# Kernel tuning notes

Hardware: AMD Instinct MI355X
Metric: run time of the kernel (lower is better)

## Reference

```python
import math
import jax, jax.numpy as jnp
import numpy as np

B, C_IN, H, W = 16, 384, 64, 64
CDIM, K, NSCALES, ITERS = 128, 64, 2, 3

def conv1x1(x, w, b):
    # x: [B,C,H,W], w: [O,C], b: [O]
    return jnp.einsum('bchw,oc->bohw', x, w) + b[None, :, None, None]

def mlp2(x, w1, b1, w2, b2):
    return conv1x1(jax.nn.relu(conv1x1(x, w1, b1)), w2, b2)

def log_optimal_transport(scores, dustbin, iters):
    B_, K_, N_ = scores.shape
    Z = jnp.concatenate([scores, dustbin], axis=1)  # [B,K+1,N]
    log_mu = jnp.full((B_, K_ + 1), -math.log(K_ + 1), dtype=scores.dtype)
    log_nu = jnp.full((B_, N_), -math.log(N_), dtype=scores.dtype)
    u = jnp.zeros_like(log_mu)
    v = jnp.zeros_like(log_nu)
    for _ in range(iters):
        u = log_mu - jax.nn.logsumexp(Z + v[:, None, :], axis=2)
        v = log_nu - jax.nn.logsumexp(Z + u[:, :, None], axis=1)
    return Z + u[:, :, None] + v[:, None, :]

def avg_pool2(x):
    b, c, h, w = x.shape
    return x.reshape(b, c, h // 2, 2, w // 2, 2).mean(axis=(3, 5))

def scale_branch(xs, fw1, fb1, fw2, fb2, sw1, sb1, sw2, sb2, dw1, db1, dw2, db2):
    b = xs.shape[0]
    local_feat = mlp2(xs, fw1, fb1, fw2, fb2).reshape(b, CDIM, -1)   # [B,C,N]
    score = mlp2(xs, sw1, sb1, sw2, sb2).reshape(b, K, -1)           # [B,K,N]
    dustbin = mlp2(xs, dw1, db1, dw2, db2).reshape(b, 1, -1)         # [B,1,N]
    log_p = log_optimal_transport(score, dustbin, ITERS)
    p = jnp.exp(log_p)[:, :-1, :]                                    # drop dustbin row
    p = p / (p.sum(axis=-1, keepdims=True) + 1e-8)
    out = jnp.einsum('bcn,bkn->bck', local_feat, p)                  # [B,C,K]
    out = out / jnp.clip(jnp.linalg.norm(out, axis=1, keepdims=True), 1e-12)
    return out.reshape(b, -1), local_feat

def setup_inputs():
    key = jax.random.key(0)
    ks = jax.random.split(key, 13)
    inp = {'x': jax.random.normal(ks[0], (B, C_IN, H, W), jnp.float32)}
    kidx = 1
    for s in range(NSCALES):
        for name, (o, i) in [('fw1', (512, C_IN)), ('fw2', (CDIM, 512)),
                              ('sw1', (512, C_IN)), ('sw2', (K, 512)),
                              ('dw1', (128, C_IN)), ('dw2', (1, 128))]:
            inp[f'{name}_{s}'] = 0.02 * jax.random.normal(ks[kidx % 13], (o, i), jnp.float32)
            inp[f'{name[0]}b{name[2]}_{s}'] = jnp.zeros((o,), jnp.float32)
            kidx += 1
    return inp

def reference(x,
              fw1_0, fb1_0, fw2_0, fb2_0, sw1_0, sb1_0, sw2_0, sb2_0, dw1_0, db1_0, dw2_0, db2_0,
              fw1_1, fb1_1, fw2_1, fb2_1, sw1_1, sb1_1, sw2_1, sb2_1, dw1_1, db1_1, dw2_1, db2_1):
    params = [
        (fw1_0, fb1_0, fw2_0, fb2_0, sw1_0, sb1_0, sw2_0, sb2_0, dw1_0, db1_0, dw2_0, db2_0),
        (fw1_1, fb1_1, fw2_1, fb2_1, sw1_1, sb1_1, sw2_1, sb2_1, dw1_1, db1_1, dw2_1, db2_1),
    ]
    descs = []
    xs = x
    for s in range(NSCALES):
        if s > 0:
            xs = avg_pool2(xs)
        d, _ = scale_branch(xs, *params[s])
        descs.append(d)
    g = jnp.stack(descs, axis=1).mean(axis=1)
    g = g / jnp.clip(jnp.linalg.norm(g, axis=1, keepdims=True), 1e-12)
    return g
```

## Files before the change

### kernel.cpp

```cpp
#include <hip/hip_runtime.h>
#include <math.h>

typedef __attribute__((ext_vector_type(8))) short short8;
typedef __attribute__((ext_vector_type(4))) float floatx4;

__device__ inline float bf2f(short s) {
    union { unsigned u; float f; } x; x.u = ((unsigned)(unsigned short)s) << 16; return x.f;
}
__device__ inline short f2bf(float f) {
    union { float f; unsigned u; } x; x.f = f;
    unsigned r = x.u + 0x7fff + ((x.u >> 16) & 1);
    return (short)(r >> 16);
}

struct WSet {
    const float *fw1, *fb1, *fw2, *sw1, *sb1, *sw2, *sb2, *dw1, *db1, *dw2, *db2;
};

__global__ __launch_bounds__(256) void wprep(WSet a0, WSet a1,
    short* __restrict__ W1f, short* __restrict__ W2af, short* __restrict__ W2bf,
    float* __restrict__ B1p, float* __restrict__ B2bp)
{
    const int s = blockIdx.y;
    const WSet A = s ? a1 : a0;
    W1f  += (size_t)s * 491520;
    W2af += (size_t)s * 65536;
    W2bf += (size_t)s * 98304;
    B1p  += s * 1280;
    B2bp += s * 128;
    int id = blockIdx.x * 256 + threadIdx.x;
    if (id < 491520) {
        int e = id & 7, l = (id >> 3) & 63, g = (id >> 9) & 15, rest = id >> 13;
        int kc = rest % 12, c = rest / 12;
        int m = c * 256 + g * 16 + (l & 15);
        int k = kc * 32 + (l >> 4) * 8 + e;
        float v = 0.f;
        if (m < 512) v = A.fw1[m * 384 + k];
        else if (m < 1024) v = A.sw1[(m - 512) * 384 + k];
        else if (m < 1152) v = A.dw1[(m - 1024) * 384 + k];
        W1f[id] = f2bf(v);
        return;
    }
    id -= 491520;
    if (id < 65536) {
        int e = id & 7, l = (id >> 3) & 63, g = (id >> 9) & 7, ka = id >> 12;
        int r = g * 16 + (l & 15), k = ka * 32 + (l >> 4) * 8 + e;
        W2af[id] = f2bf(A.fw2[r * 512 + k]);
        return;
    }
    id -= 65536;
    if (id < 98304) {
        int e = id & 7, l = (id >> 3) & 63, g = (id >> 9) & 7, kb = id >> 12;
        int r = g * 16 + (l & 15), krel = kb * 32 + (l >> 4) * 8 + e;
        float v = 0.f;
        if (r < 64 && krel < 512) v = A.sw2[r * 512 + krel];
        else if (r == 64 && krel >= 512 && krel < 640) v = A.dw2[krel - 512];
        W2bf[id] = f2bf(v);
        return;
    }
    id -= 98304;
    if (id < 1280) {
        float v = 0.f;
        if (id < 512) v = A.fb1[id];
        else if (id < 1024) v = A.sb1[id - 512];
        else if (id < 1152) v = A.db1[id - 1024];
        B1p[id] = v;
        return;
    }
    id -= 1280;
    if (id < 128) B2bp[id] = id < 64 ? A.sb2[id] : id == 64 ? A.db2[0] : 0.f;
}

__global__ __launch_bounds__(256) void xprep(const float* __restrict__ x,
                                             short* __restrict__ xT, short* __restrict__ x1T)
{
    __shared__ float xt[64 * 129];
    const int ip = blockIdx.x;
    const int cg = blockIdx.y;
    const int b  = blockIdx.z;
    const int t  = threadIdx.x;
    #pragma unroll
    for (int u = 0; u < 32; u++) {
        int idx = t + 256 * u;
        int c = idx >> 7, sp = idx & 127;
        xt[c * 129 + sp] = x[(((long)b * 384 + cg * 64 + c) * 64 + ip * 2 + (sp >> 6)) * 64 + (sp & 63)];
    }
    __syncthreads();
    {
        int sp = t >> 1, ch = t & 1;
        short tmp[32];
        #pragma unroll
        for (int cc = 0; cc < 32; cc++) tmp[cc] = f2bf(xt[(ch * 32 + cc) * 129 + sp]);
        short* dst = xT + ((long)b * 4096 + ip * 128 + sp) * 384 + cg * 64 + ch * 32;
        #pragma unroll
        for (int v = 0; v < 4; v++) *(short8*)(dst + v * 8) = *(short8*)(tmp + v * 8);
    }
    {
        int j1 = t >> 3, c8 = t & 7;
        short tmp[8];
        #pragma unroll
        for (int e = 0; e < 8; e++) {
            int c = c8 * 8 + e;
            float v = 0.25f * (xt[c * 129 + j1 * 2]      + xt[c * 129 + j1 * 2 + 1] +
                               xt[c * 129 + 64 + j1 * 2] + xt[c * 129 + 64 + j1 * 2 + 1]);
            tmp[e] = f2bf(v);
        }
        *(short8*)(x1T + ((long)b * 1024 + ip * 32 + j1) * 384 + cg * 64 + c8 * 8) = *(short8*)tmp;
    }
}

__global__ __launch_bounds__(256, 2) void fused_mlp(
    const short* __restrict__ W1f_, const float* __restrict__ B1p_,
    const short* __restrict__ W2af_, const float* __restrict__ fb2_0, const float* __restrict__ fb2_1,
    const short* __restrict__ W2bf_, const float* __restrict__ B2bp_,
    const short* __restrict__ xT, const short* __restrict__ x1T,
    float* __restrict__ feat0, float* __restrict__ feat1,
    short* __restrict__ Eg0, short* __restrict__ Eg1,
    float* __restrict__ pu0, float* __restrict__ pu1)
{
    __shared__ short xs[12 * 2048];
    __shared__ short hs[8 * 2048];
    const int tid = threadIdx.x;
    const int wid = tid >> 6, lane = tid & 63;
    const int l15 = lane & 15, q = lane >> 4;
    const int bx = blockIdx.x, b = blockIdx.y;
    const int sc = bx >= 64;
    const int tile = sc ? bx - 64 : bx;
    const int N = sc ? 1024 : 4096;
    const int n0 = tile * 64;
    const short* XT = sc ? x1T : xT;
    const short* W1f = W1f_ + (size_t)sc * 491520;
    const float* B1p = B1p_ + sc * 1280;
    const short* W2af = W2af_ + (size_t)sc * 65536;
    const short* W2bf = W2bf_ + (size_t)sc * 98304;
    const float* fb2 = sc ? fb2_1 : fb2_0;
    const float* B2bp = B2bp_ + sc * 128;
    float* feat = (sc ? feat1 : feat0) + (long)b * 128 * N;
    short* Eg = (sc ? Eg1 : Eg0) + (long)b * 65 * N;
    float* pu = sc ? pu1 : pu0;
    const int npart = sc ? 16 : 64;

    {
        const int n = tid >> 2;
        const int c0 = (tid & 3) * 12;
        const short* src = XT + ((long)b * N + n0 + n) * 384 + c0 * 8;
        const int jj = n >> 4, nl = n & 15;
        #pragma unroll
        for (int i = 0; i < 12; i++) {
            int c = c0 + i;
            int kc = c >> 2, qq = c & 3;
            *(short8*)(xs + kc * 2048 + jj * 512 + ((qq << 4) | nl) * 8) =
                *(const short8*)(src + i * 8);
        }
    }
    __syncthreads();

    floatx4 acc2[4][4];
    #pragma unroll
    for (int i = 0; i < 4; i++)
        #pragma unroll
        for (int j = 0; j < 4; j++) acc2[i][j] = floatx4{0.f, 0.f, 0.f, 0.f};

    auto phase2 = [&](int pc) {
        if (pc < 2) {
            const short* WA = W2af + (size_t)pc * 32768;
            short8 hb[2][4], wa0[2], wa1[2];
            #pragma unroll
            for (int j = 0; j < 4; j++) hb[0][j] = *(short8*)(hs + j * 512 + lane * 8);
            wa0[0] = *(const short8*)(WA + (2 * wid) * 512 + lane * 8);
            wa1[0] = *(const short8*)(WA + (2 * wid + 1) * 512 + lane * 8);
            #pragma unroll
            for (int kc2 = 0; kc2 < 8; kc2++) {
                short8 bfr[4];
                #pragma unroll
                for (int j = 0; j < 4; j++) bfr[j] = hb[kc2 & 1][j];
                short8 aA = wa0[kc2 & 1], aB = wa1[kc2 & 1];
                if (kc2 + 1 < 8) {
                    #pragma unroll
                    for (int j = 0; j < 4; j++)
                        hb[(kc2 + 1) & 1][j] = *(short8*)(hs + (kc2 + 1) * 2048 + j * 512 + lane * 8);
                    wa0[(kc2 + 1) & 1] = *(const short8*)(WA + ((kc2 + 1) * 8 + 2 * wid) * 512 + lane * 8);
                    wa1[(kc2 + 1) & 1] = *(const short8*)(WA + ((kc2 + 1) * 8 + 2 * wid + 1) * 512 + lane * 8);
                }
                #pragma unroll
                for (int j = 0; j < 4; j++) {
                    acc2[0][j] = __builtin_amdgcn_mfma_f32_16x16x32_bf16(aA, bfr[j], acc2[0][j], 0, 0, 0);
                    acc2[1][j] = __builtin_amdgcn_mfma_f32_16x16x32_bf16(aB, bfr[j], acc2[1][j], 0, 0, 0);
                }
            }
        } else {
            const short* WB = W2bf + (size_t)(pc - 2) * 32768;
            short8 hb[2][4], wc[2], wd[2];
            #pragma unroll
            for (int j = 0; j < 4; j++) hb[0][j] = *(short8*)(hs + j * 512 + lane * 8);
            wc[0] = *(const short8*)(WB + wid * 512 + lane * 8);
            wd[0] = *(const short8*)(WB + 4 * 512 + lane * 8);
            #pragma unroll
            for (int kc2 = 0; kc2 < 8; kc2++) {
                short8 bfr[4];
                #pragma unroll
                for (int j = 0; j < 4; j++) bfr[j] = hb[kc2 & 1][j];
                short8 aC = wc[kc2 & 1], aD = wd[kc2 & 1];
                if (kc2 + 1 < 8) {
                    #pragma unroll
                    for (int j = 0; j < 4; j++)
                        hb[(kc2 + 1) & 1][j] = *(short8*)(hs + (kc2 + 1) * 2048 + j * 512 + lane * 8);
                    wc[(kc2 + 1) & 1] = *(const short8*)(WB + ((kc2 + 1) * 8 + wid) * 512 + lane * 8);
                    wd[(kc2 + 1) & 1] = *(const short8*)(WB + ((kc2 + 1) * 8 + 4) * 512 + lane * 8);
                }
                #pragma unroll
                for (int j = 0; j < 4; j++)
                    acc2[2][j] = __builtin_amdgcn_mfma_f32_16x16x32_bf16(aC, bfr[j], acc2[2][j], 0, 0, 0);
                if (wid == 0) {
                    #pragma unroll
                    for (int j = 0; j < 4; j++)
                        acc2[3][j] = __builtin_amdgcn_mfma_f32_16x16x32_bf16(aD, bfr[j], acc2[3][j], 0, 0, 0);
                }
            }
        }
    };

    for (int c = 0; c < 5; c++) {
        floatx4 acc1[4][4];
        #pragma unroll
        for (int i = 0; i < 4; i++)
            #pragma unroll
            for (int j = 0; j < 4; j++) acc1[i][j] = floatx4{0.f, 0.f, 0.f, 0.f};
        const short* Wb = W1f + (long)c * 98304;
        short8 abuf[2][4], bbuf[2][4];
        #pragma unroll
        for (int i = 0; i < 4; i++) {
            abuf[0][i] = *(const short8*)(Wb + (wid * 4 + i) * 512 + lane * 8);
            abuf[1][i] = *(const short8*)(Wb + (16 + wid * 4 + i) * 512 + lane * 8);
        }
        #pragma unroll
        for (int j = 0; j < 4; j++) bbuf[0][j] = *(short8*)(xs + j * 512 + lane * 8);
        #pragma unroll
        for (int kc = 0; kc < 12; kc++) {
            short8 ac[4], bc[4];
            #pragma unroll
            for (int i = 0; i < 4; i++) ac[i] = abuf[kc & 1][i];
            #pragma unroll
            for (int j = 0; j < 4; j++) bc[j] = bbuf[kc & 1][j];
            if (kc + 2 < 12) {
                #pragma unroll
                for (int i = 0; i < 4; i++)
                    abuf[kc & 1][i] = *(const short8*)(Wb + ((kc + 2) * 16 + wid * 4 + i) * 512 + lane * 8);
            }
            if (kc + 1 < 12) {
                #pragma unroll
                for (int j = 0; j < 4; j++)
                    bbuf[(kc + 1) & 1][j] = *(short8*)(xs + (kc + 1) * 2048 + j * 512 + lane * 8);
            }
            #pragma unroll
            for (int i = 0; i < 4; i++)
                #pragma unroll
                for (int j = 0; j < 4; j++)
                    acc1[i][j] = __builtin_amdgcn_mfma_f32_16x16x32_bf16(ac[i], bc[j], acc1[i][j], 0, 0, 0);
        }
        if (c > 0) phase2(c - 1);
        __syncthreads();
        #pragma unroll
        for (int i = 0; i < 4; i++) {
            const int kc2 = wid * 2 + (i >> 1);
            const int qf = (i & 1) * 2 + (q >> 1);
            const int e0 = 4 * (q & 1);
            const int mrow = c * 256 + wid * 64 + i * 16 + q * 4;
            float bw[4];
            #pragma unroll
            for (int rr = 0; rr < 4; rr++) bw[rr] = B1p[mrow + rr];
            #pragma unroll
            for (int j = 0; j < 4; j++) {
                short pk[4];
                #pragma unroll
                for (int rr = 0; rr < 4; rr++)
                    pk[rr] = f2bf(fmaxf(acc1[i][j][rr] + bw[rr], 0.f));
                *(unsigned long long*)(hs + kc2 * 2048 + j * 512 + ((qf << 4) | l15) * 8 + e0) =
                    *(unsigned long long*)pk;
            }
        }
        __syncthreads();
    }
    phase2(4);

    #pragma unroll
    for (int slot = 0; slot < 2; slot++) {
        int row0 = (2 * wid + slot) * 16 + q * 4;
        #pragma unroll
        for (int rr = 0; rr < 4; rr++) {
            float bv = fb2[row0 + rr];
            #pragma unroll
            for (int j = 0; j < 4; j++)
                feat[(long)(row0 + rr) * N + n0 + 16 * j + l15] = acc2[slot][j][rr] + bv;
        }
    }
    __syncthreads();
    float* puld = (float*)hs;
    #pragma unroll
    for (int rr = 0; rr < 4; rr++) {
        int row = wid * 16 + q * 4 + rr;
        float bv = B2bp[row];
        float s = 0.f;
        #pragma unroll
        for (int j = 0; j < 4; j++) {
            float e = expf(acc2[2][j][rr] + bv);
            Eg[(long)row * N + n0 + 16 * j + l15] = f2bf(e);
            s += e;
        }
        s += __shfl_xor(s, 1); s += __shfl_xor(s, 2);
        s += __shfl_xor(s, 4); s += __shfl_xor(s, 8);
        if (l15 == 0) puld[row] = s;
    }
    if (wid == 0) {
        #pragma unroll
        for (int rr = 0; rr < 4; rr++) {
            int row = 64 + q * 4 + rr;
            bool valid = (row == 64);
            float bv = B2bp[64];
            float s = 0.f;
            #pragma unroll
            for (int j = 0; j < 4; j++) {
                float e = expf(acc2[3][j][rr] + bv);
                if (valid) {
                    Eg[(long)64 * N + n0 + 16 * j + l15] = f2bf(e);
                    s += e;
                }
            }
            s += __shfl_xor(s, 1); s += __shfl_xor(s, 2);
            s += __shfl_xor(s, 4); s += __shfl_xor(s, 8);
            if (valid && l15 == 0) puld[64] = s;
        }
    }
    __syncthreads();
    if (tid < 65)
        pu[((long)b * npart + tile) * 65 + tid] = puld[tid];
}

__global__ __launch_bounds__(256) void sk_step(
    const short* __restrict__ Eg0, const short* __restrict__ Eg1,
    const float* __restrict__ pin0, const float* __restrict__ pin1,
    float* __restrict__ pout0, float* __restrict__ pout1, int nin0, int nin1)
{
    __shared__ short Es[65 * 264];
    __shared__ float evs[256];
    __shared__ float eus[65];
    const int t = threadIdx.x;
    const int bx = blockIdx.x, b = blockIdx.y;
    const int sc = bx >= 16;
    const int chunk = sc ? bx - 16 : bx;
    const int N = sc ? 1024 : 4096;
    const float invN = sc ? (1.0f / 1024.0f) : (1.0f / 4096.0f);
    const int n0 = chunk * 256;
    const short* Eb = (sc ? Eg1 : Eg0) + (long)b * 65 * N;
    const float* pin = sc ? pin1 : pin0;
    const int nin = sc ? nin1 : nin0;
    float* pout = sc ? pout1 : pout0;
    const int nout = sc ? 4 : 16;
    if (t < 65) {
        float s = 0.f;
        for (int ch = 0; ch < nin; ch++) s += pin[((long)b * nin + ch) * 65 + t];
        eus[t] = (1.0f / 65.0f) / s;
    }
    for (int it = t; it < 2080; it += 256) {
        int k = it >> 5, n8 = it & 31;
        *(short8*)(Es + k * 264 + n8 * 8) = *(const short8*)(Eb + (long)k * N + n0 + n8 * 8);
    }
    __syncthreads();
    float sv = 0.f;
    #pragma unroll 4
    for (int k = 0; k < 65; k++) sv += bf2f(Es[k * 264 + t]) * eus[k];
    evs[t] = invN / sv;
    __syncthreads();
    const int wid = t >> 6, lane = t & 63;
    for (int k = wid; k < 65; k += 4) {
        const short* er = Es + k * 264 + lane * 4;
        float4 v4 = *(const float4*)&evs[lane * 4];
        float s = bf2f(er[0]) * v4.x + bf2f(er[1]) * v4.y + bf2f(er[2]) * v4.z + bf2f(er[3]) * v4.w;
        #pragma unroll
        for (int off = 32; off >= 1; off >>= 1) s += __shfl_xor(s, off);
        if (lane == 0) pout[((long)b * nout + chunk) * 65 + k] = s;
    }
}

__global__ __launch_bounds__(256) void sk_desc(
    const short* __restrict__ Eg0, const short* __restrict__ Eg1,
    const float* __restrict__ pin0, const float* __restrict__ pin1,
    const float* __restrict__ feat0, const float* __restrict__ feat1,
    float* __restrict__ part0, float* __restrict__ part1, int nin0, int nin1)
{
    __shared__ short Es[65 * 264];
    __shared__ float eus[65];
    const int t = threadIdx.x;
    const int bx = blockIdx.x, b = blockIdx.y;
    const int sc = bx >= 16;
    const int chunk = sc ? bx - 16 : bx;
    const int N = sc ? 1024 : 4096;
    const float invN = sc ? (1.0f / 1024.0f) : (1.0f / 4096.0f);
    const int nch = sc ? 4 : 16;
    const int n0 = chunk * 256;
    const short* Eb = (sc ? Eg1 : Eg0) + (long)b * 65 * N;
    const float* pin = sc ? pin1 : pin0;
    const int nin = sc ? nin1 : nin0;
    const float* fb = (sc ? feat1 : feat0) + (long)b * 128 * N;
    float* part = sc ? part1 : part0;
    if (t < 65) {
        float s = 0.f;
        for (int ch = 0; ch < nin; ch++) s += pin[((long)b * nin + ch) * 65 + t];
        eus[t] = (1.0f / 65.0f) / s;
    }
    for (int it = t; it < 2080; it += 256) {
        int k = it >> 5, n8 = it & 31;
        *(short8*)(Es + k * 264 + n8 * 8) = *(const short8*)(Eb + (long)k * N + n0 + n8 * 8);
    }
    __syncthreads();
    float sv = 0.f;
    #pragma unroll 4
    for (int k = 0; k < 65; k++) sv += bf2f(Es[k * 264 + t]) * eus[k];
    float evt = invN / sv;
    #pragma unroll 4
    for (int k = 0; k < 64; k++)
        Es[k * 264 + t] = f2bf(bf2f(Es[k * 264 + t]) * eus[k] * evt);
    __syncthreads();
    const int wid = t >> 6, lane = t & 63;
    const int l15 = lane & 15, q = lane >> 4;
    float* pb = part + ((long)b * nch + chunk) * 8256;
    for (int k = wid; k < 64; k += 4) {
        const short* er = Es + k * 264 + lane * 4;
        float s = bf2f(er[0]) + bf2f(er[1]) + bf2f(er[2]) + bf2f(er[3]);
        #pragma unroll
        for (int off = 32; off >= 1; off >>= 1) s += __shfl_xor(s, off);
        if (lane == 0) pb[8192 + k] = s;
    }
    floatx4 acc[2][4];
    #pragma unroll
    for (int mt = 0; mt < 2; mt++)
        #pragma unroll
        for (int nt = 0; nt < 4; nt++) acc[mt][nt] = floatx4{0.f, 0.f, 0.f, 0.f};
    #pragma unroll 2
    for (int ks = 0; ks < 8; ks++) {
        short8 ah[2], al[2];
        #pragma unroll
        for (int mt = 0; mt < 2; mt++) {
            const float* fp = fb + (long)(wid * 32 + mt * 16 + l15) * N + n0 + ks * 32 + q * 8;
            float4 v0 = *(const float4*)fp;
            float4 v1 = *(const float4*)(fp + 4);
            float va[8] = {v0.x, v0.y, v0.z, v0.w, v1.x, v1.y, v1.z, v1.w};
            short hh[8], ll[8];
            #pragma unroll
            for (int e = 0; e < 8; e++) {
                short h = f2bf(va[e]);
                hh[e] = h;
                ll[e] = f2bf(va[e] - bf2f(h));
            }
            ah[mt] = *(short8*)hh;
            al[mt] = *(short8*)ll;
        }
        #pragma unroll
        for (int nt = 0; nt < 4; nt++) {
            short8 bfr = *(short8*)(Es + (nt * 16 + l15) * 264 + ks * 32 + q * 8);
            #pragma unroll
            for (int mt = 0; mt < 2; mt++) {
                acc[mt][nt] = __builtin_amdgcn_mfma_f32_16x16x32_bf16(al[mt], bfr, acc[mt][nt], 0, 0, 0);
                acc[mt][nt] = __builtin_amdgcn_mfma_f32_16x16x32_bf16(ah[mt], bfr, acc[mt][nt], 0, 0, 0);
            }
        }
    }
    #pragma unroll
    for (int mt = 0; mt < 2; mt++)
        #pragma unroll
        for (int nt = 0; nt < 4; nt++)
            #pragma unroll
            for (int rr = 0; rr < 4; rr++)
                pb[(wid * 32 + mt * 16 + q * 4 + rr) * 64 + nt * 16 + l15] = acc[mt][nt][rr];
}

__global__ __launch_bounds__(256) void desc_reduce(
    const float* __restrict__ part0, const float* __restrict__ part1,
    float* __restrict__ desc0, float* __restrict__ desc1, int b0)
{
    __shared__ float cred[4][8];
    const int bx = blockIdx.x, b = blockIdx.y;
    const int sc = bx >= 4;
    const int kg = (bx & 3) * 16;
    const int nch = sc ? 4 : 16;
    const float* pb = (sc ? part1 : part0) + (long)b * nch * 8256;
    float* desc = sc ? desc1 : desc0;
    const int t = threadIdx.x;
    const int c = t & 127, kh = t >> 7;
    float a[8], rs[8];
    #pragma unroll
    for (int j = 0; j < 8; j++) { a[j] = 0.f; rs[j] = 0.f; }
    for (int ch = 0; ch < nch; ch++) {
        const float* p = pb + (long)ch * 8256;
        #pragma unroll
        for (int j = 0; j < 8; j++) a[j] += p[c * 64 + kg + kh * 8 + j];
        #pragma unroll
        for (int j = 0; j < 8; j++) rs[j] += p[8192 + kg + kh * 8 + j];
    }
    float sq[8];
    #pragma unroll
    for (int j = 0; j < 8; j++) {
        a[j] *= 1.0f / (rs[j] + 1e-8f);
        sq[j] = a[j] * a[j];
    }
    #pragma unroll
    for (int off = 32; off >= 1; off >>= 1)
        #pragma unroll
        for (int j = 0; j < 8; j++) sq[j] += __shfl_xor(sq[j], off);
    if ((t & 63) == 0) {
        #pragma unroll
        for (int j = 0; j < 8; j++) cred[t >> 6][j] = sq[j];
    }
    __syncthreads();
    float* d = desc + (long)(b0 + b) * 8192;
    #pragma unroll
    for (int j = 0; j < 8; j++) {
        float tot = cred[kh * 2][j] + cred[kh * 2 + 1][j];
        float inv = 1.0f / fmaxf(sqrtf(tot), 1e-12f);
        d[c * 64 + kg + kh * 8 + j] = a[j] * inv;
    }
}

__global__ __launch_bounds__(256) void final_kernel(const float* __restrict__ desc0,
                                                    const float* __restrict__ desc1,
                                                    float* __restrict__ out)
{
    __shared__ float red[4];
    const int b = blockIdx.x;
    const float* d0 = desc0 + (long)b * 8192;
    const float* d1 = desc1 + (long)b * 8192;
    float s = 0;
    for (int i = threadIdx.x; i < 8192; i += 256) {
        float t = (d0[i] + d1[i]) * 0.5f; s += t * t;
    }
    const int wave = threadIdx.x >> 6, lane = threadIdx.x & 63;
    #pragma unroll
    for (int off = 32; off >= 1; off >>= 1) s += __shfl_xor(s, off);
    if (lane == 0) red[wave] = s;
    __syncthreads();
    float tot = red[0] + red[1] + red[2] + red[3];
    float inv = 1.0f / fmaxf(sqrtf(tot), 1e-12f);
    for (int i = threadIdx.x; i < 8192; i += 256)
        out[(long)b * 8192 + i] = (d0[i] + d1[i]) * 0.5f * inv;
}

extern "C" void kernel_launch(void* const* d_in, const int* in_sizes, int n_in,
                              void* d_out, int out_size, void* d_ws, size_t ws_size,
                              hipStream_t stream)
{
    (void)in_sizes; (void)n_in; (void)out_size;
    const float* x = (const float*)d_in[0];
    WSet ws2[2];
    const float* fb2p[2];
    for (int s = 0; s < 2; s++) {
        int o = 1 + s * 12;
        ws2[s].fw1 = (const float*)d_in[o + 0];  ws2[s].fb1 = (const float*)d_in[o + 1];
        ws2[s].fw2 = (const float*)d_in[o + 2];  fb2p[s]    = (const float*)d_in[o + 3];
        ws2[s].sw1 = (const float*)d_in[o + 4];  ws2[s].sb1 = (const float*)d_in[o + 5];
        ws2[s].sw2 = (const float*)d_in[o + 6];  ws2[s].sb2 = (const float*)d_in[o + 7];
        ws2[s].dw1 = (const float*)d_in[o + 8];  ws2[s].db1 = (const float*)d_in[o + 9];
        ws2[s].dw2 = (const float*)d_in[o + 10]; ws2[s].db2 = (const float*)d_in[o + 11];
    }

    const size_t fixed = ((size_t)2*491520*2 + 2*65536*2 + 2*98304*2
                        + 2*1280*4 + 2*128*4 + (size_t)2*16*8192*4) + (1 << 16);
    const size_t perb = (size_t)4096*384*2 + (size_t)1024*384*2
                      + (size_t)128*4096*4 + (size_t)128*1024*4
                      + (size_t)65*4096*2 + (size_t)65*1024*2
                      + (size_t)(64+16)*65*4 + (size_t)(16+4)*65*4
                      + (size_t)16*8256*4 + (size_t)4*8256*4 + 8192;
    int CB = 4;
    const int cand[3] = {16, 8, 4};
    for (int ci = 0; ci < 3; ci++)
        if (fixed + (size_t)cand[ci] * perb <= ws_size) { CB = cand[ci]; break; }

    char* p = (char*)d_ws;
    auto alloc = [&](size_t bytes) -> char* {
        char* r = p; p += (bytes + 255) & ~(size_t)255; return r;
    };
    short* W1f   = (short*)alloc((size_t)2 * 491520 * 2);
    short* W2af  = (short*)alloc((size_t)2 * 65536 * 2);
    short* W2bf  = (short*)alloc((size_t)2 * 98304 * 2);
    float* B1p   = (float*)alloc((size_t)2 * 1280 * 4);
    float* B2bp  = (float*)alloc((size_t)2 * 128 * 4);
    float* desc0 = (float*)alloc((size_t)16 * 8192 * 4);
    float* desc1 = (float*)alloc((size_t)16 * 8192 * 4);
    short* xT    = (short*)alloc((size_t)CB * 4096 * 384 * 2);
    short* x1T   = (short*)alloc((size_t)CB * 1024 * 384 * 2);
    float* feat0 = (float*)alloc((size_t)CB * 128 * 4096 * 4);
    float* feat1 = (float*)alloc((size_t)CB * 128 * 1024 * 4);
    short* Eg0   = (short*)alloc((size_t)CB * 65 * 4096 * 2);
    short* Eg1   = (short*)alloc((size_t)CB * 65 * 1024 * 2);
    float* puA0  = (float*)alloc((size_t)CB * 64 * 65 * 4);
    float* puA1  = (float*)alloc((size_t)CB * 16 * 65 * 4);
    float* puB0  = (float*)alloc((size_t)CB * 16 * 65 * 4);
    float* puB1  = (float*)alloc((size_t)CB * 4 * 65 * 4);
    float* part0 = (float*)alloc((size_t)CB * 16 * 8256 * 4);
    float* part1 = (float*)alloc((size_t)CB * 4 * 8256 * 4);

    wprep<<<dim3(2566, 2), 256, 0, stream>>>(ws2[0], ws2[1], W1f, W2af, W2bf, B1p, B2bp);

    for (int b0 = 0; b0 < 16; b0 += CB) {
        xprep<<<dim3(32, 6, CB), 256, 0, stream>>>(x + (size_t)b0 * 384 * 4096, xT, x1T);
        fused_mlp<<<dim3(80, CB), 256, 0, stream>>>(
            W1f, B1p, W2af, fb2p[0], fb2p[1], W2bf, B2bp,
            xT, x1T, feat0, feat1, Eg0, Eg1, puA0, puA1);
        sk_step<<<dim3(20, CB), 256, 0, stream>>>(Eg0, Eg1, puA0, puA1, puB0, puB1, 64, 16);
        sk_step<<<dim3(20, CB), 256, 0, stream>>>(Eg0, Eg1, puB0, puB1, puA0, puA1, 16, 4);
        sk_desc<<<dim3(20, CB), 256, 0, stream>>>(Eg0, Eg1, puA0, puA1,
                                                  feat0, feat1, part0, part1, 16, 4);
        desc_reduce<<<dim3(8, CB), 256, 0, stream>>>(part0, part1, desc0, desc1, b0);
    }
    final_kernel<<<16, 256, 0, stream>>>(desc0, desc1, (float*)d_out);
}
```

Measured before the change: 470.8 us.

## Use 512-thread blocks in fused MLP and vectorize xprep loads

The fused MLP kernel now runs 8 waves per block instead of 4, with each wave computing half as many output rows, so per-wave accumulator state drops and more waves can hide latency. The phase-2 GEMM for the previous chunk is moved ahead of the phase-1 GEMM, and the LDS double-buffering of the x tiles is replaced by direct per-iteration loads. xprep now reads x with float4 loads. In exchange, several waves sit idle in the score/dustbin phase, and the launch bound of 512 threads with 4 blocks per CU may cap registers or be unreachable given the LDS footprint.

```diff
diff --git a/kernel.cpp b/kernel.cpp
--- a/kernel.cpp
+++ b/kernel.cpp
@@ -80,10 +80,12 @@
     const int b  = blockIdx.z;
     const int t  = threadIdx.x;
     #pragma unroll
-    for (int u = 0; u < 32; u++) {
+    for (int u = 0; u < 8; u++) {
         int idx = t + 256 * u;
-        int c = idx >> 7, sp = idx & 127;
-        xt[c * 129 + sp] = x[(((long)b * 384 + cg * 64 + c) * 64 + ip * 2 + (sp >> 6)) * 64 + (sp & 63)];
+        int c = idx >> 5, spq = idx & 31;
+        float4 v = *(const float4*)&x[(((long)b * 384 + cg * 64 + c) * 64 + ip * 2 + (spq >> 4)) * 64 + (spq & 15) * 4];
+        float* d = &xt[c * 129 + spq * 4];
+        d[0] = v.x; d[1] = v.y; d[2] = v.z; d[3] = v.w;
     }
     __syncthreads();
     {
@@ -109,7 +111,7 @@
     }
 }
 
-__global__ __launch_bounds__(256, 2) void fused_mlp(
+__global__ __launch_bounds__(512, 4) void fused_mlp(
     const short* __restrict__ W1f_, const float* __restrict__ B1p_,
     const short* __restrict__ W2af_, const float* __restrict__ fb2_0, const float* __restrict__ fb2_1,
     const short* __restrict__ W2bf_, const float* __restrict__ B2bp_,
@@ -141,12 +143,12 @@
     const int npart = sc ? 16 : 64;
 
     {
-        const int n = tid >> 2;
-        const int c0 = (tid & 3) * 12;
+        const int n = tid >> 3;
+        const int c0 = (tid & 7) * 6;
         const short* src = XT + ((long)b * N + n0 + n) * 384 + c0 * 8;
         const int jj = n >> 4, nl = n & 15;
         #pragma unroll
-        for (int i = 0; i < 12; i++) {
+        for (int i = 0; i < 6; i++) {
             int c = c0 + i;
             int kc = c >> 2, qq = c & 3;
             *(short8*)(xs + kc * 2048 + jj * 512 + ((qq << 4) | nl) * 8) =
@@ -155,117 +157,99 @@
     }
     __syncthreads();
 
-    floatx4 acc2[4][4];
-    #pragma unroll
-    for (int i = 0; i < 4; i++)
+    floatx4 acc2[2][4];
+    #pragma unroll
+    for (int i = 0; i < 2; i++)
         #pragma unroll
         for (int j = 0; j < 4; j++) acc2[i][j] = floatx4{0.f, 0.f, 0.f, 0.f};
 
     auto phase2 = [&](int pc) {
         if (pc < 2) {
             const short* WA = W2af + (size_t)pc * 32768;
-            short8 hb[2][4], wa0[2], wa1[2];
+            short8 hb[2][4], wa[2];
             #pragma unroll
             for (int j = 0; j < 4; j++) hb[0][j] = *(short8*)(hs + j * 512 + lane * 8);
-            wa0[0] = *(const short8*)(WA + (2 * wid) * 512 + lane * 8);
-            wa1[0] = *(const short8*)(WA + (2 * wid + 1) * 512 + lane * 8);
+            wa[0] = *(const short8*)(WA + wid * 512 + lane * 8);
             #pragma unroll
             for (int kc2 = 0; kc2 < 8; kc2++) {
                 short8 bfr[4];
                 #pragma unroll
                 for (int j = 0; j < 4; j++) bfr[j] = hb[kc2 & 1][j];
-                short8 aA = wa0[kc2 & 1], aB = wa1[kc2 & 1];
+                short8 aF = wa[kc2 & 1];
                 if (kc2 + 1 < 8) {
                     #pragma unroll
                     for (int j = 0; j < 4; j++)
                         hb[(kc2 + 1) & 1][j] = *(short8*)(hs + (kc2 + 1) * 2048 + j * 512 + lane * 8);
-                    wa0[(kc2 + 1) & 1] = *(const short8*)(WA + ((kc2 + 1) * 8 + 2 * wid) * 512 + lane * 8);
-                    wa1[(kc2 + 1) & 1] = *(const short8*)(WA + ((kc2 + 1) * 8 + 2 * wid + 1) * 512 + lane * 8);
+                    wa[(kc2 + 1) & 1] = *(const short8*)(WA + ((kc2 + 1) * 8 + wid) * 512 + lane * 8);
                 }
                 #pragma unroll
-                for (int j = 0; j < 4; j++) {
-                    acc2[0][j] = __builtin_amdgcn_mfma_f32_16x16x32_bf16(aA, bfr[j], acc2[0][j], 0, 0, 0);
-                    acc2[1][j] = __builtin_amdgcn_mfma_f32_16x16x32_bf16(aB, bfr[j], acc2[1][j], 0, 0, 0);
-                }
+                for (int j = 0; j < 4; j++)
+                    acc2[0][j] = __builtin_amdgcn_mfma_f32_16x16x32_bf16(aF, bfr[j], acc2[0][j], 0, 0, 0);
             }
         } else {
+            if (wid >= 5) return;
             const short* WB = W2bf + (size_t)(pc - 2) * 32768;
-            short8 hb[2][4], wc[2], wd[2];
+            short8 hb[2][4], we[2];
             #pragma unroll
             for (int j = 0; j < 4; j++) hb[0][j] = *(short8*)(hs + j * 512 + lane * 8);
-            wc[0] = *(const short8*)(WB + wid * 512 + lane * 8);
-            wd[0] = *(const short8*)(WB + 4 * 512 + lane * 8);
+            we[0] = *(const short8*)(WB + wid * 512 + lane * 8);
             #pragma unroll
             for (int kc2 = 0; kc2 < 8; kc2++) {
                 short8 bfr[4];
                 #pragma unroll
                 for (int j = 0; j < 4; j++) bfr[j] = hb[kc2 & 1][j];
-                short8 aC = wc[kc2 & 1], aD = wd[kc2 & 1];
+                short8 aE = we[kc2 & 1];
                 if (kc2 + 1 < 8) {
                     #pragma unroll
                     for (int j = 0; j < 4; j++)
                         hb[(kc2 + 1) & 1][j] = *(short8*)(hs + (kc2 + 1) * 2048 + j * 512 + lane * 8);
-                    wc[(kc2 + 1) & 1] = *(const short8*)(WB + ((kc2 + 1) * 8 + wid) * 512 + lane * 8);
-                    wd[(kc2 + 1) & 1] = *(const short8*)(WB + ((kc2 + 1) * 8 + 4) * 512 + lane * 8);
+                    we[(kc2 + 1) & 1] = *(const short8*)(WB + ((kc2 + 1) * 8 + wid) * 512 + lane * 8);
                 }
                 #pragma unroll
                 for (int j = 0; j < 4; j++)
-                    acc2[2][j] = __builtin_amdgcn_mfma_f32_16x16x32_bf16(aC, bfr[j], acc2[2][j], 0, 0, 0);
-                if (wid == 0) {
-                    #pragma unroll
-                    for (int j = 0; j < 4; j++)
-                        acc2[3][j] = __builtin_amdgcn_mfma_f32_16x16x32_bf16(aD, bfr[j], acc2[3][j], 0, 0, 0);
-                }
+                    acc2[1][j] = __builtin_amdgcn_mfma_f32_16x16x32_bf16(aE, bfr[j], acc2[1][j], 0, 0, 0);
             }
         }
     };
 
     for (int c = 0; c < 5; c++) {
-        floatx4 acc1[4][4];
-        #pragma unroll
-        for (int i = 0; i < 4; i++)
+        if (c > 0) phase2(c - 1);
+        floatx4 acc1[2][4];
+        #pragma unroll
+        for (int i = 0; i < 2; i++)
             #pragma unroll
             for (int j = 0; j < 4; j++) acc1[i][j] = floatx4{0.f, 0.f, 0.f, 0.f};
         const short* Wb = W1f + (long)c * 98304;
-        short8 abuf[2][4], bbuf[2][4];
-        #pragma unroll
-        for (int i = 0; i < 4; i++) {
-            abuf[0][i] = *(const short8*)(Wb + (wid * 4 + i) * 512 + lane * 8);
-            abuf[1][i] = *(const short8*)(Wb + (16 + wid * 4 + i) * 512 + lane * 8);
-        }
-        #pragma unroll
-        for (int j = 0; j < 4; j++) bbuf[0][j] = *(short8*)(xs + j * 512 + lane * 8);
+        short8 abuf[2][2];
+        #pragma unroll
+        for (int i = 0; i < 2; i++) {
+            abuf[0][i] = *(const short8*)(Wb + (wid * 2 + i) * 512 + lane * 8);
+            abuf[1][i] = *(const short8*)(Wb + (16 + wid * 2 + i) * 512 + lane * 8);
+        }
         #pragma unroll
         for (int kc = 0; kc < 12; kc++) {
-            short8 ac[4], bc[4];
-            #pragma unroll
-            for (int i = 0; i < 4; i++) ac[i] = abuf[kc & 1][i];
-            #pragma unroll
-            for (int j = 0; j < 4; j++) bc[j] = bbuf[kc & 1][j];
+            short8 ac[2], bc[4];
+            #pragma unroll
+            for (int i = 0; i < 2; i++) ac[i] = abuf[kc & 1][i];
+            #pragma unroll
+            for (int j = 0; j < 4; j++) bc[j] = *(short8*)(xs + kc * 2048 + j * 512 + lane * 8);
             if (kc + 2 < 12) {
                 #pragma unroll
-                for (int i = 0; i < 4; i++)
-                    abuf[kc & 1][i] = *(const short8*)(Wb + ((kc + 2) * 16 + wid * 4 + i) * 512 + lane * 8);
-            }
-            if (kc + 1 < 12) {
-                #pragma unroll
-                for (int j = 0; j < 4; j++)
-                    bbuf[(kc + 1) & 1][j] = *(short8*)(xs + (kc + 1) * 2048 + j * 512 + lane * 8);
-            }
-            #pragma unroll
-            for (int i = 0; i < 4; i++)
+                for (int i = 0; i < 2; i++)
+                    abuf[kc & 1][i] = *(const short8*)(Wb + ((kc + 2) * 16 + wid * 2 + i) * 512 + lane * 8);
+            }
+            #pragma unroll
+            for (int i = 0; i < 2; i++)
                 #pragma unroll
                 for (int j = 0; j < 4; j++)
                     acc1[i][j] = __builtin_amdgcn_mfma_f32_16x16x32_bf16(ac[i], bc[j], acc1[i][j], 0, 0, 0);
         }
-        if (c > 0) phase2(c - 1);
         __syncthreads();
         #pragma unroll
-        for (int i = 0; i < 4; i++) {
-            const int kc2 = wid * 2 + (i >> 1);
-            const int qf = (i & 1) * 2 + (q >> 1);
+        for (int i = 0; i < 2; i++) {
+            const int qf = i * 2 + (q >> 1);
             const int e0 = 4 * (q & 1);
-            const int mrow = c * 256 + wid * 64 + i * 16 + q * 4;
+            const int mrow = c * 256 + wid * 32 + i * 16 + q * 4;
             float bw[4];
             #pragma unroll
             for (int rr = 0; rr < 4; rr++) bw[rr] = B1p[mrow + rr];
@@ -275,7 +259,7 @@
                 #pragma unroll
                 for (int rr = 0; rr < 4; rr++)
                     pk[rr] = f2bf(fmaxf(acc1[i][j][rr] + bw[rr], 0.f));
-                *(unsigned long long*)(hs + kc2 * 2048 + j * 512 + ((qf << 4) | l15) * 8 + e0) =
+                *(unsigned long long*)(hs + wid * 2048 + j * 512 + ((qf << 4) | l15) * 8 + e0) =
                     *(unsigned long long*)pk;
             }
         }
@@ -283,35 +267,35 @@
     }
     phase2(4);
 
-    #pragma unroll
-    for (int slot = 0; slot < 2; slot++) {
-        int row0 = (2 * wid + slot) * 16 + q * 4;
+    {
+        const int row0 = wid * 16 + q * 4;
         #pragma unroll
         for (int rr = 0; rr < 4; rr++) {
             float bv = fb2[row0 + rr];
             #pragma unroll
             for (int j = 0; j < 4; j++)
-                feat[(long)(row0 + rr) * N + n0 + 16 * j + l15] = acc2[slot][j][rr] + bv;
+                feat[(long)(row0 + rr) * N + n0 + 16 * j + l15] = acc2[0][j][rr] + bv;
         }
     }
     __syncthreads();
     float* puld = (float*)hs;
-    #pragma unroll
-    for (int rr = 0; rr < 4; rr++) {
-        int row = wid * 16 + q * 4 + rr;
-        float bv = B2bp[row];
-        float s = 0.f;
-        #pragma unroll
-        for (int j = 0; j < 4; j++) {
-            float e = expf(acc2[2][j][rr] + bv);
-            Eg[(long)row * N + n0 + 16 * j + l15] = f2bf(e);
-            s += e;
-        }
-        s += __shfl_xor(s, 1); s += __shfl_xor(s, 2);
-        s += __shfl_xor(s, 4); s += __shfl_xor(s, 8);
-        if (l15 == 0) puld[row] = s;
-    }
-    if (wid == 0) {
+    if (wid < 4) {
+        #pragma unroll
+        for (int rr = 0; rr < 4; rr++) {
+            int row = wid * 16 + q * 4 + rr;
+            float bv = B2bp[row];
+            float s = 0.f;
+            #pragma unroll
+            for (int j = 0; j < 4; j++) {
+                float e = expf(acc2[1][j][rr] + bv);
+                Eg[(long)row * N + n0 + 16 * j + l15] = f2bf(e);
+                s += e;
+            }
+            s += __shfl_xor(s, 1); s += __shfl_xor(s, 2);
+            s += __shfl_xor(s, 4); s += __shfl_xor(s, 8);
+            if (l15 == 0) puld[row] = s;
+        }
+    } else if (wid == 4) {
         #pragma unroll
         for (int rr = 0; rr < 4; rr++) {
             int row = 64 + q * 4 + rr;
@@ -320,7 +304,7 @@
             float s = 0.f;
             #pragma unroll
             for (int j = 0; j < 4; j++) {
-                float e = expf(acc2[3][j][rr] + bv);
+                float e = expf(acc2[1][j][rr] + bv);
                 if (valid) {
                     Eg[(long)64 * N + n0 + 16 * j + l15] = f2bf(e);
                     s += e;
@@ -602,7 +586,7 @@
 
     for (int b0 = 0; b0 < 16; b0 += CB) {
         xprep<<<dim3(32, 6, CB), 256, 0, stream>>>(x + (size_t)b0 * 384 * 4096, xT, x1T);
-        fused_mlp<<<dim3(80, CB), 256, 0, stream>>>(
+        fused_mlp<<<dim3(80, CB), 512, 0, stream>>>(
             W1f, B1p, W2af, fb2p[0], fb2p[1], W2bf, B2bp,
             xT, x1T, feat0, feat1, Eg0, Eg1, puA0, puA1);
         sk_step<<<dim3(20, CB), 256, 0, stream>>>(Eg0, Eg1, puA0, puA1, puB0, puB1, 64, 16);
```

Result: faster. 395.1 us (-16.1%).
